# Kernel optimization log

Measured on AMD Instinct MI355X. Metric: run time of the kernel, lower is better.

## Reference

```python
import jax, jax.numpy as jnp
import numpy as np


def conv2d(x, w, bias, stride=1, pad=0, groups=1):
    out = jax.lax.conv_general_dilated(
        x, w, (stride, stride), [(pad, pad), (pad, pad)],
        dimension_numbers=("NCHW", "OIHW", "NCHW"), feature_group_count=groups)
    return out + bias[None, :, None, None]


PATCHSIZE = [(4, 4), (8, 8)]
NEG = jnp.float32(-1e9)


def setup_inputs() -> dict:
    key = jax.random.key(0)
    ks = jax.random.split(key, 24)
    d = 128
    s = 0.05
    inp = {
        "x": jax.random.normal(ks[0], (16, d, 64, 64), jnp.float32),
        "m": jax.random.uniform(ks[1], (16, 1, 64, 64), jnp.float32),
        "depth_map": jax.random.normal(ks[2], (16, 1, 256, 256), jnp.float32),
        "wq": jax.random.normal(ks[3], (d, d, 1, 1), jnp.float32) * s,
        "bq": jax.random.normal(ks[4], (d,), jnp.float32) * s,
        "wk": jax.random.normal(ks[5], (d, d, 1, 1), jnp.float32) * s,
        "bk": jax.random.normal(ks[6], (d,), jnp.float32) * s,
        "wv": jax.random.normal(ks[7], (d, d, 1, 1), jnp.float32) * s,
        "bv": jax.random.normal(ks[8], (d,), jnp.float32) * s,
        "wvle": jax.random.normal(ks[9], (d, 1, 3, 3), jnp.float32) * s,  # depthwise
        "bvle": jax.random.normal(ks[10], (d,), jnp.float32) * s,
        "wd1": jax.random.normal(ks[11], (d, 1, 3, 3), jnp.float32) * s,
        "bd1": jax.random.normal(ks[12], (d,), jnp.float32) * s,
        "wd2": jax.random.normal(ks[13], (1, d, 3, 3), jnp.float32) * s,
        "bd2": jax.random.normal(ks[14], (1,), jnp.float32) * s,
        "wo": jax.random.normal(ks[15], (d, d, 3, 3), jnp.float32) * s,
        "bo": jax.random.normal(ks[16], (d,), jnp.float32) * s,
        "b": 2,
        "c": 128,
    }
    return inp


def _forward(x, m, depth_map, wq, bq, wk, bk, wv, bv, wvle, bvle,
             wd1, bd1, wd2, bd2, wo, bo, b, c):
    bt, _, h, w = x.shape
    t = bt // b
    d_k = c // len(PATCHSIZE)

    q_all = conv2d(x, wq, bq)
    k_all = conv2d(x, wk, bk)
    v_all = conv2d(x, wv, bv) + conv2d(x, wvle, bvle, pad=1, groups=c)
    d1 = jax.nn.relu(conv2d(depth_map, wd1, bd1, stride=2, pad=1))
    _depth = jax.nn.relu(conv2d(d1, wd2, bd2, stride=2, pad=1))  # (bt,1,h,w)

    outs = []
    for i, (width, height) in enumerate(PATCHSIZE):
        out_w, out_h = w // width, h // height
        L = t * out_h * out_w

        def patch(z, ch):
            # (b*t, ch, h, w) -> (b, L, ch*height*width)
            z = z.reshape(b, t, ch, out_h, height, out_w, width)
            return z.transpose(0, 1, 3, 5, 2, 4, 6).reshape(b, L, ch * height * width)

        mask = jnp.mean(patch(m, 1), -1) > 0.5            # (b, L) per-key mask
        dsort = jnp.sort(patch(_depth, 1), -1)            # (b, L, height*width)
        hw = height * width
        dmin, dmed, dmax = dsort[..., 0], dsort[..., (hw - 1) // 2], dsort[..., -1]

        q = patch(q_all[:, i * d_k:(i + 1) * d_k], d_k)
        k_ = patch(k_all[:, i * d_k:(i + 1) * d_k], d_k)
        v = patch(v_all[:, i * d_k:(i + 1) * d_k], d_k)

        scale = 1.0 / jnp.sqrt(jnp.float32(q.shape[-1]))
        s = jnp.einsum("bqd,bkd->bqk", q, k_) * scale     # shared QK^T

        def head(dbias):
            ss = s * jax.nn.sigmoid(dbias)[:, None, :]
            ss = jnp.where(mask[:, None, :], NEG, ss)
            return jnp.einsum("bqk,bkd->bqd", jax.nn.softmax(ss, -1), v)

        y = (head(dmed) + head(dmax) + head(dmin)) / 3.0
        y = y.reshape(b, t, out_h, out_w, d_k, height, width)
        y = y.transpose(0, 1, 4, 2, 5, 3, 6).reshape(bt, d_k, h, w)
        outs.append(y)

    out = jnp.concatenate(outs, 1)
    out = conv2d(out, wo, bo, pad=1)
    out = jnp.where(out >= 0, out, 0.2 * out)  # LeakyReLU(0.2)
    return out


def reference(x, m, depth_map, wq, bq, wk, bk, wv, bv, wvle, bvle,
              wd1, bd1, wd2, bd2, wo, bo, b, c):
    out = _forward(x, m, depth_map, wq, bq, wk, bk, wv, bv, wvle, bvle,
                   wd1, bd1, wd2, bd2, wo, bo, b, c)
    return (out, depth_map)
```

## Files before the change

kernel.cpp:

```cpp
#include <hip/hip_runtime.h>
#include <cmath>

typedef unsigned short u16;
typedef __attribute__((ext_vector_type(8))) __bf16 bf16x8;
typedef __attribute__((ext_vector_type(4))) float f32x4;

constexpr int Bb = 2, Tt = 8, Dc = 128, PIX = 4096;

__device__ inline u16 f2bf(float f) {
    unsigned u = __builtin_bit_cast(unsigned, f);
    u += 0x7fffu + ((u >> 16) & 1u);
    return (u16)(u >> 16);
}
__device__ inline float bf2f(u16 h) {
    unsigned u = ((unsigned)h) << 16;
    return __builtin_bit_cast(float, u);
}

#define GLOAD16(gp, lp) __builtin_amdgcn_global_load_lds( \
    (const __attribute__((address_space(1))) void*)(const void*)(gp), \
    (__attribute__((address_space(3))) void*)(void*)(lp), 16, 0, 0)

__device__ inline void mfma_chunk(const u16* lAs, const u16* lBs, int wave, int lane,
                                  f32x4 (&acc)[4][4])
{
    const int wm = (wave >> 1) * 64, wn = (wave & 1) * 64;
    const int fr = lane & 15;
    const int q4 = lane >> 4;
    const int sw = (q4 ^ ((fr >> 1) & 3)) * 8;
    bf16x8 av[4], bv[4];
#pragma unroll
    for (int i = 0; i < 4; ++i) av[i] = *(const bf16x8*)&lAs[(wm + i * 16 + fr) * 32 + sw];
#pragma unroll
    for (int j = 0; j < 4; ++j) bv[j] = *(const bf16x8*)&lBs[(wn + j * 16 + fr) * 32 + sw];
#pragma unroll
    for (int i = 0; i < 4; ++i)
#pragma unroll
        for (int j = 0; j < 4; ++j)
            acc[i][j] = __builtin_amdgcn_mfma_f32_16x16x32_bf16(av[i], bv[j], acc[i][j], 0, 0, 0);
}

__device__ inline void stage_chunk(const u16* ga0, const u16* ga1,
                                   const u16* gb0, const u16* gb1,
                                   int kb, u16* lA, u16* lB, int wave)
{
    GLOAD16(ga0 + kb * 32, lA + wave * 1024);
    GLOAD16(ga1 + kb * 32, lA + wave * 1024 + 512);
    GLOAD16(gb0 + kb * 32, lB + wave * 1024);
    GLOAD16(gb1 + kb * 32, lB + wave * 1024 + 512);
}

__device__ inline void mfma_nt(const u16* A, int ldkA, const u16* B, int ldkB,
                               int kChunks, int wave, int lane,
                               u16* lAs, u16* lBs, f32x4 (&acc)[4][4])
{
    const int r = lane >> 2;
    const int kq8 = ((lane & 3) ^ ((r >> 1) & 3)) * 8;
    const u16* ga0 = A + (size_t)(wave * 32 + r) * ldkA + kq8;
    const u16* ga1 = ga0 + (size_t)16 * ldkA;
    const u16* gb0 = B + (size_t)(wave * 32 + r) * ldkB + kq8;
    const u16* gb1 = gb0 + (size_t)16 * ldkB;
    stage_chunk(ga0, ga1, gb0, gb1, 0, lAs, lBs, wave);
    __syncthreads();
    for (int kb = 0; kb < kChunks; ++kb) {
        if (kb + 1 < kChunks) {
            const int nx = ((kb + 1) & 1) * 4096;
            stage_chunk(ga0, ga1, gb0, gb1, kb + 1, lAs + nx, lBs + nx, wave);
        }
        const int cur = (kb & 1) * 4096;
        mfma_chunk(lAs + cur, lBs + cur, wave, lane, acc);
        __syncthreads();
    }
}

__global__ void k_prep(const float* __restrict__ wq, const float* __restrict__ wk,
                       const float* __restrict__ wv, const float* __restrict__ wo,
                       u16* __restrict__ Wqkv, u16* __restrict__ WoT)
{
    int idx = blockIdx.x * 256 + threadIdx.x;
    if (idx < 49152) {
        const float* w = idx < 16384 ? wq : (idx < 32768 ? wk : wv);
        Wqkv[idx] = f2bf(w[idx & 16383]);
    }
    int j = idx - 49152;
    if (j >= 0 && j < 147456) {
        int tap = j / 16384, rem = j % 16384;
        WoT[j] = f2bf(wo[(size_t)rem * 9 + tap]);
    }
}

__global__ __launch_bounds__(256) void k_xt(const float* __restrict__ x, u16* __restrict__ Xt)
{
    __shared__ float ls[128 * 65];
    const int n = blockIdx.y, pix0 = blockIdx.x * 64;
#pragma unroll
    for (int rep = 0; rep < 32; ++rep) {
        int idx = rep * 256 + threadIdx.x;
        int cin = idx >> 6, p = idx & 63;
        ls[cin * 65 + p] = x[((size_t)n * Dc + cin) * PIX + pix0 + p];
    }
    __syncthreads();
#pragma unroll
    for (int rep = 0; rep < 32; ++rep) {
        int idx = rep * 256 + threadIdx.x;
        int p = idx >> 7, cin = idx & 127;
        Xt[((size_t)n * PIX + pix0 + p) * Dc + cin] = f2bf(ls[cin * 65 + p]);
    }
}

__global__ __launch_bounds__(256) void k_qkv_mfma(const u16* __restrict__ Wqkv,
                                                  const u16* __restrict__ Xt,
                                                  const float* __restrict__ bq,
                                                  const float* __restrict__ bk,
                                                  const float* __restrict__ bv,
                                                  u16* __restrict__ Qp0, u16* __restrict__ Kp0,
                                                  u16* __restrict__ Qp1, u16* __restrict__ Kp1,
                                                  u16* __restrict__ v_bf)
{
    __shared__ u16 lAs[8192], lBs[8192];
    const int tid = threadIdx.x, wave = tid >> 6, lane = tid & 63;
    const int mt = blockIdx.y, n = blockIdx.z, px0 = blockIdx.x * 128;
    f32x4 acc[4][4];
#pragma unroll
    for (int i = 0; i < 4; ++i)
#pragma unroll
        for (int j = 0; j < 4; ++j) acc[i][j] = (f32x4){0.f, 0.f, 0.f, 0.f};
    mfma_nt(Wqkv + (size_t)mt * 128 * 128, 128,
            Xt + ((size_t)n * PIX + px0) * 128, 128, 4, wave, lane, lAs, lBs, acc);
    const int wm = (wave >> 1) * 64, wn = (wave & 1) * 64;
    const int rb = (lane >> 4) * 4, cb = lane & 15;
    const int bi = n >> 3, ti = n & 7;
    if (mt < 2) {
        const float* bp = (mt == 0) ? bq : bk;
        u16* d0 = (mt == 0) ? Qp0 : Kp0;
        u16* d1 = (mt == 0) ? Qp1 : Kp1;
#pragma unroll
        for (int i = 0; i < 4; ++i)
#pragma unroll
            for (int reg = 0; reg < 4; ++reg) {
                int c = wm + i * 16 + rb + reg;
                float bias = bp[c];
#pragma unroll
                for (int j = 0; j < 4; ++j) {
                    int pix = px0 + wn + j * 16 + cb;
                    int y = pix >> 6, x = pix & 63;
                    u16 val = f2bf(acc[i][j][reg] + bias);
                    if (c < 64) {
                        int l = ti * 256 + (y >> 2) * 16 + (x >> 2);
                        int f = c * 16 + (y & 3) * 4 + (x & 3);
                        d0[((size_t)bi * 2048 + l) * 1024 + f] = val;
                    } else {
                        int l = ti * 64 + (y >> 3) * 8 + (x >> 3);
                        int f = (c - 64) * 64 + (y & 7) * 8 + (x & 7);
                        d1[((size_t)bi * 512 + l) * 4096 + f] = val;
                    }
                }
            }
    } else {
#pragma unroll
        for (int i = 0; i < 4; ++i)
#pragma unroll
            for (int reg = 0; reg < 4; ++reg) {
                int c = wm + i * 16 + rb + reg;
                float bias = bv[c];
#pragma unroll
                for (int j = 0; j < 4; ++j) {
                    int pix = px0 + wn + j * 16 + cb;
                    v_bf[((size_t)n * Dc + c) * PIX + pix] = f2bf(acc[i][j][reg] + bias);
                }
            }
    }
}

__global__ __launch_bounds__(256) void k_fuse(const float* __restrict__ X,
                                              const float* __restrict__ wvle,
                                              const float* __restrict__ bvle,
                                              const u16* __restrict__ v_bf,
                                              u16* __restrict__ Vt0,
                                              u16* __restrict__ Vt1,
                                              const float* __restrict__ dm,
                                              const float* __restrict__ wd1,
                                              const float* __restrict__ bd1,
                                              const float* __restrict__ wd2,
                                              float* __restrict__ part)
{
    __shared__ float ls[4096];
    __shared__ u16 lv[64 * 65];
    const int id = blockIdx.x;
    const int sub = id >> 1;
    const int tid = threadIdx.x;
    if ((id & 1) == 0) {
        const int c = sub & 127, n = sub >> 7;
        const int bi = n >> 3, ti = n & 7;
        const float* xp = X + ((size_t)n * Dc + c) * PIX;
#pragma unroll
        for (int r = 0; r < 4; ++r)
            *(float4*)&ls[r * 1024 + tid * 4] = *(const float4*)&xp[r * 1024 + tid * 4];
        __syncthreads();
        float w[9];
#pragma unroll
        for (int t = 0; t < 9; ++t) w[t] = wvle[c * 9 + t];
        const float bias = bvle[c];
        const int x = tid & 63, y0 = (tid >> 6) * 16;
        const bool xl = (x > 0), xr = (x < 63);
        const u16* vp = v_bf + ((size_t)n * Dc + c) * PIX;
#pragma unroll
        for (int r = 0; r < 16; ++r) {
            int y = y0 + r;
            float s = bias;
#pragma unroll
            for (int ky = 0; ky < 3; ++ky) {
                int yy = y + ky - 1;
                if (yy < 0 || yy > 63) continue;
                const float* row = &ls[yy * 64];
                float m   = row[x];
                float lv_ = xl ? row[x - 1] : 0.f;
                float rv  = xr ? row[x + 1] : 0.f;
                s += w[ky * 3 + 0] * lv_ + w[ky * 3 + 1] * m + w[ky * 3 + 2] * rv;
            }
            lv[y * 65 + x] = f2bf(bf2f(vp[y * 64 + x]) + s);
        }
        __syncthreads();
        if (c < 64) {
            const int fsub = tid >> 4;
            const int py = fsub >> 2, px = fsub & 3;
            const int oh = tid & 15;
            u16 buf[16];
#pragma unroll
            for (int ow = 0; ow < 16; ++ow)
                buf[ow] = lv[(oh * 4 + py) * 65 + ow * 4 + px];
            size_t dst = ((size_t)bi * 1024 + (c * 16 + fsub)) * 2048 + ti * 256 + oh * 16;
            *(uint4*)&Vt0[dst]     = *(const uint4*)&buf[0];
            *(uint4*)&Vt0[dst + 8] = *(const uint4*)&buf[8];
        } else {
            const int fsub = tid >> 2;
            const int py = fsub >> 3, px = fsub & 7;
            const int l0 = (tid & 3) * 16;
            u16 buf[16];
#pragma unroll
            for (int e = 0; e < 16; ++e) {
                int l = l0 + e, oh = l >> 3, ow = l & 7;
                buf[e] = lv[(oh * 8 + py) * 65 + ow * 8 + px];
            }
            size_t dst = ((size_t)bi * 4096 + ((c - 64) * 64 + fsub)) * 512 + ti * 64 + l0;
            *(uint4*)&Vt1[dst]     = *(const uint4*)&buf[0];
            *(uint4*)&Vt1[dst + 8] = *(const uint4*)&buf[8];
        }
    } else {
        const int tile = sub & 15, n = (sub >> 4) & 15, cs = sub >> 8;
        const int ty = tid >> 4, tx = tid & 15;
        const int y = (tile >> 2) * 16 + ty;
        const int x = (tile & 3) * 16 + tx;
        const float* dmp = dm + (size_t)n * 65536;
        const int gc0 = 4 * x - 4;
        const bool vy = (y > 0), vx = (x > 0);
        const int c0 = cs * 16;
        float acc = 0.f;
#pragma unroll 1
        for (int jy = 0; jy < 3; ++jy) {
            float rw[3][7];
#pragma unroll
            for (int rr = 0; rr < 3; ++rr) {
                const int gr = 4 * y - 3 + 2 * jy + rr;
                const float* rp = dmp + gr * 256 + gc0;
                const bool rok = (gr >= 0);
                float4 va = (rok && x > 0) ? *(const float4*)rp
                                           : make_float4(0.f, 0.f, 0.f, 0.f);
                float4 vb = rok ? *(const float4*)(rp + 4)
                                : make_float4(0.f, 0.f, 0.f, 0.f);
                rw[rr][0] = va.y; rw[rr][1] = va.z; rw[rr][2] = va.w;
                rw[rr][3] = vb.x; rw[rr][4] = vb.y; rw[rr][5] = vb.z; rw[rr][6] = vb.w;
            }
#pragma unroll
            for (int rr = 0; rr < 3; ++rr)
#pragma unroll
                for (int i = 0; i < 7; ++i) asm volatile("" : "+v"(rw[rr][i]));
            const bool oky = (jy > 0) || vy;
#pragma unroll 2
            for (int cc = 0; cc < 16; ++cc) {
                const int c = c0 + cc;
                const float* w1 = wd1 + c * 9;
                const float* w2 = wd2 + c * 9 + jy * 3;
                const float b1 = bd1[c];
#pragma unroll
                for (int jx = 0; jx < 3; ++jx) {
                    float s = b1;
#pragma unroll
                    for (int ky = 0; ky < 3; ++ky)
#pragma unroll
                        for (int kx = 0; kx < 3; ++kx)
                            s += w1[ky * 3 + kx] * rw[ky][2 * jx + kx];
                    s = fmaxf(s, 0.f);
                    const bool ok = oky && ((jx > 0) || vx);
                    acc += w2[jx] * (ok ? s : 0.f);
                }
            }
        }
        part[((size_t)cs * 16 + n) * PIX + y * 64 + x] = acc;
    }
}

__global__ void k_dfin(const float* __restrict__ part, const float* __restrict__ bd2,
                       float* __restrict__ dep)
{
    int idx = blockIdx.x * 256 + threadIdx.x;
    float s = bd2[0];
#pragma unroll
    for (int cg = 0; cg < 8; ++cg) s += part[(size_t)cg * 65536 + idx];
    dep[idx] = fmaxf(s, 0.f);
}

template<int PS>
__global__ __launch_bounds__(256) void k_stats2(const float* __restrict__ mI,
                                                const float* __restrict__ dep,
                                                float* __restrict__ maskf,
                                                float* __restrict__ smed,
                                                float* __restrict__ smaxA,
                                                float* __restrict__ sminA,
                                                int outn, int L)
{
    constexpr int HW = PS * PS;
    constexpr int TPB = 256 / HW;
    const int tok = blockIdx.x * TPB + threadIdx.x / HW;
    const int el  = threadIdx.x % HW;
    if (tok >= Bb * L) return;
    const int bi = tok / L, l = tok % L;
    const int ti = l / (outn * outn); const int rem = l % (outn * outn);
    const int oh = rem / outn, ow = rem % outn;
    const int n = bi * Tt + ti;
    const int py = el / PS, px = el % PS;
    const size_t off = (size_t)n * PIX + (size_t)(oh * PS + py) * 64 + ow * PS + px;
    const float mv = mI[off];
    const float dv = dep[off];
    float msum = mv, vmin = dv, vmax = dv;
#pragma unroll
    for (int o = HW / 2; o > 0; o >>= 1) {
        msum += __shfl_xor(msum, o);
        vmin = fminf(vmin, __shfl_xor(vmin, o));
        vmax = fmaxf(vmax, __shfl_xor(vmax, o));
    }
    const int gbase = (threadIdx.x & 63) & ~(HW - 1);
    int cl = 0, ce = 0;
#pragma unroll
    for (int b2 = 0; b2 < HW; ++b2) {
        float vb = __shfl(dv, gbase + b2);
        cl += (vb < dv);
        ce += (vb == dv);
    }
    constexpr int kk = (HW - 1) / 2;
    if (el == 0) {
        maskf[tok] = (msum / (float)HW > 0.5f) ? 1.f : 0.f;
        smaxA[tok] = 1.f / (1.f + __expf(-vmax));
        sminA[tok] = 1.f / (1.f + __expf(-vmin));
    }
    if (cl <= kk && kk < cl + ce)
        smed[tok] = 1.f / (1.f + __expf(-dv));
}

__global__ __launch_bounds__(256) void k_qkT_mfma(const u16* __restrict__ Qp,
                                                  const u16* __restrict__ Kp,
                                                  u16* __restrict__ S,
                                                  int L, int F, int ksplit, float scale)
{
    __shared__ u16 lAs[8192], lBs[8192];
    const int tid = threadIdx.x, wave = tid >> 6, lane = tid & 63;
    const int bi = blockIdx.z / ksplit, ks = blockIdx.z % ksplit;
    const int kf = F / ksplit;
    f32x4 acc[4][4];
#pragma unroll
    for (int i = 0; i < 4; ++i)
#pragma unroll
        for (int j = 0; j < 4; ++j) acc[i][j] = (f32x4){0.f, 0.f, 0.f, 0.f};
    mfma_nt(Qp + (size_t)bi * L * F + (size_t)blockIdx.y * 128 * F + (size_t)ks * kf, F,
            Kp + (size_t)bi * L * F + (size_t)blockIdx.x * 128 * F + (size_t)ks * kf, F,
            kf / 32, wave, lane, lAs, lBs, acc);
    const int wm = (wave >> 1) * 64, wn = (wave & 1) * 64;
    const int rb = (lane >> 4) * 4, cb = lane & 15;
    u16* Cp = S + ((size_t)ks * Bb + bi) * L * L;
#pragma unroll
    for (int i = 0; i < 4; ++i)
#pragma unroll
        for (int reg = 0; reg < 4; ++reg) {
            int gm = blockIdx.y * 128 + wm + i * 16 + rb + reg;
#pragma unroll
            for (int j = 0; j < 4; ++j) {
                int gn = blockIdx.x * 128 + wn + j * 16 + cb;
                Cp[(size_t)gm * L + gn] = f2bf(acc[i][j][reg] * scale);
            }
        }
}

__device__ inline float blockMax(float v, float* sh) {
#pragma unroll
    for (int o = 32; o > 0; o >>= 1) v = fmaxf(v, __shfl_down(v, o));
    __syncthreads();
    if ((threadIdx.x & 63) == 0) sh[threadIdx.x >> 6] = v;
    __syncthreads();
    return fmaxf(fmaxf(sh[0], sh[1]), fmaxf(sh[2], sh[3]));
}
__device__ inline float blockSum(float v, float* sh) {
#pragma unroll
    for (int o = 32; o > 0; o >>= 1) v += __shfl_down(v, o);
    __syncthreads();
    if ((threadIdx.x & 63) == 0) sh[threadIdx.x >> 6] = v;
    __syncthreads();
    return sh[0] + sh[1] + sh[2] + sh[3];
}

template<int NPAIR, int NSPLIT>
__global__ __launch_bounds__(256) void k_softmax(const u16* __restrict__ S,
                                                 u16* __restrict__ Pb,
                                                 const float* __restrict__ maskf,
                                                 const float* __restrict__ smed,
                                                 const float* __restrict__ smaxA,
                                                 const float* __restrict__ sminA,
                                                 int L)
{
    __shared__ float sred[4];
    const int bi = blockIdx.y, q = blockIdx.x;
    const size_t pstr = (size_t)Bb * L * L;
    const u16* row = S + (size_t)bi * L * L + (size_t)q * L;
    u16* prow = Pb + (size_t)bi * L * L + (size_t)q * L;
    const float* mk  = maskf + bi * L;
    const float* s0p = smed  + bi * L;
    const float* s1p = smaxA + bi * L;
    const float* s2p = sminA + bi * L;
    const int tid = threadIdx.x;
    float a0[2 * NPAIR], a1[2 * NPAIR], a2[2 * NPAIR];
    float m0 = -3.4e38f, m1 = -3.4e38f, m2 = -3.4e38f;
#pragma unroll
    for (int e = 0; e < NPAIR; ++e) {
        int k = e * 512 + tid * 2;
        unsigned u = *(const unsigned*)&row[k];
        float sva = bf2f((u16)(u & 0xffffu));
        float svb = bf2f((u16)(u >> 16));
#pragma unroll
        for (int s2 = 1; s2 < NSPLIT; ++s2) {
            unsigned w = *(const unsigned*)&row[(size_t)s2 * pstr + k];
            sva += bf2f((u16)(w & 0xffffu));
            svb += bf2f((u16)(w >> 16));
        }
        float2 mv  = *(const float2*)&mk[k];
        float2 p0  = *(const float2*)&s0p[k];
        float2 p1  = *(const float2*)&s1p[k];
        float2 p2  = *(const float2*)&s2p[k];
        bool ma = mv.x > 0.5f, mb = mv.y > 0.5f;
        float v0a = ma ? -1e9f : sva * p0.x, v0b = mb ? -1e9f : svb * p0.y;
        float v1a = ma ? -1e9f : sva * p1.x, v1b = mb ? -1e9f : svb * p1.y;
        float v2a = ma ? -1e9f : sva * p2.x, v2b = mb ? -1e9f : svb * p2.y;
        a0[2 * e] = v0a; a0[2 * e + 1] = v0b;
        a1[2 * e] = v1a; a1[2 * e + 1] = v1b;
        a2[2 * e] = v2a; a2[2 * e + 1] = v2b;
        m0 = fmaxf(m0, fmaxf(v0a, v0b));
        m1 = fmaxf(m1, fmaxf(v1a, v1b));
        m2 = fmaxf(m2, fmaxf(v2a, v2b));
    }
    m0 = blockMax(m0, sred); m1 = blockMax(m1, sred); m2 = blockMax(m2, sred);
    float l0 = 0.f, l1 = 0.f, l2 = 0.f;
#pragma unroll
    for (int e = 0; e < 2 * NPAIR; ++e) {
        a0[e] = __expf(a0[e] - m0); l0 += a0[e];
        a1[e] = __expf(a1[e] - m1); l1 += a1[e];
        a2[e] = __expf(a2[e] - m2); l2 += a2[e];
    }
    l0 = blockSum(l0, sred); l1 = blockSum(l1, sred); l2 = blockSum(l2, sred);
    float c0 = 1.f / (3.f * l0), c1 = 1.f / (3.f * l1), c2 = 1.f / (3.f * l2);
#pragma unroll
    for (int e = 0; e < NPAIR; ++e) {
        int k = e * 512 + tid * 2;
        u16 oa = f2bf(a0[2 * e] * c0 + a1[2 * e] * c1 + a2[2 * e] * c2);
        u16 ob = f2bf(a0[2 * e + 1] * c0 + a1[2 * e + 1] * c1 + a2[2 * e + 1] * c2);
        unsigned pk = (unsigned)oa | ((unsigned)ob << 16);
        *(unsigned*)&prow[k] = pk;
    }
}

__global__ __launch_bounds__(256) void k_pv_mfma(const u16* __restrict__ Pb,
                                                 const u16* __restrict__ Vt,
                                                 u16* __restrict__ Yp,
                                                 int L, int F, int ksplit)
{
    __shared__ u16 lAs[8192], lBs[8192];
    const int tid = threadIdx.x, wave = tid >> 6, lane = tid & 63;
    const int bi = blockIdx.z / ksplit, ks = blockIdx.z % ksplit;
    const int kf = L / ksplit;
    f32x4 acc[4][4];
#pragma unroll
    for (int i = 0; i < 4; ++i)
#pragma unroll
        for (int j = 0; j < 4; ++j) acc[i][j] = (f32x4){0.f, 0.f, 0.f, 0.f};
    mfma_nt(Pb + (size_t)bi * L * L + (size_t)blockIdx.y * 128 * L + (size_t)ks * kf, L,
            Vt + (size_t)bi * F * L + (size_t)blockIdx.x * 128 * L + (size_t)ks * kf, L,
            kf / 32, wave, lane, lAs, lBs, acc);
    const int wm = (wave >> 1) * 64, wn = (wave & 1) * 64;
    const int rb = (lane >> 4) * 4, cb = lane & 15;
    u16* Cp = Yp + ((size_t)(ks * Bb + bi) * L) * F;
#pragma unroll
    for (int i = 0; i < 4; ++i)
#pragma unroll
        for (int reg = 0; reg < 4; ++reg) {
            int gm = blockIdx.y * 128 + wm + i * 16 + rb + reg;
#pragma unroll
            for (int j = 0; j < 4; ++j) {
                int gn = blockIdx.x * 128 + wn + j * 16 + cb;
                Cp[(size_t)gm * F + gn] = f2bf(acc[i][j][reg]);
            }
        }
}

template<int NSPLIT>
__global__ void k_unpatch(const u16* __restrict__ Yp, u16* __restrict__ catbT,
                          int ps, int outn, int L, int F, int cbase)
{
    size_t idx = (size_t)blockIdx.x * 256 + threadIdx.x;
    size_t total = (size_t)Bb * L * F / 4;
    if (idx >= total) return;
    const size_t pstr = (size_t)Bb * L * F;
    int f0 = (int)((idx * 4) % F);
    size_t t2 = (idx * 4) / F;
    int l = (int)(t2 % L);
    int bi = (int)(t2 / L);
    size_t off = ((size_t)bi * L + l) * F + f0;
    float s[4] = {0.f, 0.f, 0.f, 0.f};
#pragma unroll
    for (int sp = 0; sp < NSPLIT; ++sp) {
        uint2 u = *(const uint2*)&Yp[(size_t)sp * pstr + off];
        s[0] += bf2f((u16)(u.x & 0xffffu));
        s[1] += bf2f((u16)(u.x >> 16));
        s[2] += bf2f((u16)(u.y & 0xffffu));
        s[3] += bf2f((u16)(u.y >> 16));
    }
    int hw = ps * ps;
    int c = cbase + f0 / hw, r0 = f0 % hw;
    int ti = l / (outn * outn); int rem = l % (outn * outn);
    int oh = rem / outn, ow = rem % outn;
    int n = bi * Tt + ti;
    int py = r0 / ps, px = r0 % ps;
    size_t base = ((size_t)n * PIX + (size_t)(oh * ps + py) * 64 + ow * ps + px) * Dc + c;
#pragma unroll
    for (int e = 0; e < 4; ++e)
        catbT[base + (size_t)e * Dc] = f2bf(s[e]);
}

__global__ __launch_bounds__(256) void k_conv_mfma(const u16* __restrict__ catbT,
                                                   const u16* __restrict__ WoT,
                                                   const u16* __restrict__ zp,
                                                   u16* __restrict__ Cpart)
{
    __shared__ u16 lAs[8192], lBs[8192];
    const int tid = threadIdx.x, wave = tid >> 6, lane = tid & 63;
    const int pix0 = blockIdx.x * 128;
    const int sp = blockIdx.y;
    const int r = lane >> 2;
    const int kq8 = ((lane & 3) ^ ((r >> 1) & 3)) * 8;
    int yb[2], xb[2], nn[2];
#pragma unroll
    for (int s = 0; s < 2; ++s) {
        int pg = pix0 + wave * 32 + r + s * 16;
        nn[s] = pg >> 12; yb[s] = (pg >> 6) & 63; xb[s] = pg & 63;
    }
    const u16* gb_base = WoT + (size_t)(wave * 32 + r) * 128 + kq8;

    auto stage = [&](int tt, int hb) {
        const int t = sp * 18 + tt;
        const int tap = t >> 2, kc = t & 3;
        const int dy = tap / 3 - 1, dx = tap % 3 - 1;
        const u16* ga[2];
#pragma unroll
        for (int s = 0; s < 2; ++s) {
            int y = yb[s] + dy, xx = xb[s] + dx;
            bool ok = ((unsigned)y < 64u) && ((unsigned)xx < 64u);
            ga[s] = ok ? catbT + (((size_t)(nn[s] << 12) + y * 64 + xx) << 7) + kq8 + kc * 32 : zp;
        }
        const u16* gb = gb_base + tap * 16384 + kc * 32;
        GLOAD16(ga[0],     lAs + hb * 4096 + wave * 1024);
        GLOAD16(ga[1],     lAs + hb * 4096 + wave * 1024 + 512);
        GLOAD16(gb,        lBs + hb * 4096 + wave * 1024);
        GLOAD16(gb + 2048, lBs + hb * 4096 + wave * 1024 + 512);
    };

    f32x4 acc[4][4];
#pragma unroll
    for (int i = 0; i < 4; ++i)
#pragma unroll
        for (int j = 0; j < 4; ++j) acc[i][j] = (f32x4){0.f, 0.f, 0.f, 0.f};

    stage(0, 0);
    __syncthreads();
    for (int tt = 0; tt < 18; ++tt) {
        if (tt + 1 < 18) stage(tt + 1, (tt + 1) & 1);
        const int cur = (tt & 1) * 4096;
        mfma_chunk(lAs + cur, lBs + cur, wave, lane, acc);
        __syncthreads();
    }

    const int wm = (wave >> 1) * 64, wn = (wave & 1) * 64;
    const int rb = (lane >> 4) * 4, cb = lane & 15;
    u16* Cp = Cpart + (size_t)sp * 8388608;
#pragma unroll
    for (int i = 0; i < 4; ++i)
#pragma unroll
        for (int reg = 0; reg < 4; ++reg) {
            int gm = pix0 + wm + i * 16 + rb + reg;
#pragma unroll
            for (int j = 0; j < 4; ++j) {
                int gn = wn + j * 16 + cb;
                Cp[(size_t)gm * 128 + gn] = f2bf(acc[i][j][reg]);
            }
        }
}

__global__ __launch_bounds__(256) void k_cfin(const u16* __restrict__ Cpart,
                                              const float* __restrict__ bo,
                                              float* __restrict__ outp)
{
    const int pg0 = blockIdx.x * 64;
    const int lane = threadIdx.x & 63, wv = threadIdx.x >> 6;
    const int pix = pg0 + lane;
    const int n = pix >> 12, p = pix & 4095;
    const u16* r0 = Cpart + (size_t)pix * 128 + wv * 32;
    const u16* r1 = r0 + 8388608;
#pragma unroll
    for (int c4 = 0; c4 < 8; ++c4) {
        uint2 a = *(const uint2*)(r0 + c4 * 4);
        uint2 b = *(const uint2*)(r1 + c4 * 4);
        float s[4];
        s[0] = bf2f((u16)(a.x & 0xffffu)) + bf2f((u16)(b.x & 0xffffu));
        s[1] = bf2f((u16)(a.x >> 16))     + bf2f((u16)(b.x >> 16));
        s[2] = bf2f((u16)(a.y & 0xffffu)) + bf2f((u16)(b.y & 0xffffu));
        s[3] = bf2f((u16)(a.y >> 16))     + bf2f((u16)(b.y >> 16));
#pragma unroll
        for (int e = 0; e < 4; ++e) {
            int cout = wv * 32 + c4 * 4 + e;
            float v = s[e] + bo[cout];
            v = (v >= 0.f) ? v : 0.2f * v;
            outp[((size_t)n * Dc + cout) * PIX + p] = v;
        }
    }
}

extern "C" void kernel_launch(void* const* d_in, const int* in_sizes, int n_in,
                              void* d_out, int out_size, void* d_ws, size_t ws_size,
                              hipStream_t stream)
{
    (void)in_sizes; (void)n_in; (void)out_size; (void)ws_size;
    const float* x    = (const float*)d_in[0];
    const float* mI   = (const float*)d_in[1];
    const float* dmap = (const float*)d_in[2];
    const float* wq   = (const float*)d_in[3];
    const float* bq   = (const float*)d_in[4];
    const float* wk   = (const float*)d_in[5];
    const float* bk   = (const float*)d_in[6];
    const float* wv   = (const float*)d_in[7];
    const float* bv   = (const float*)d_in[8];
    const float* wvle = (const float*)d_in[9];
    const float* bvle = (const float*)d_in[10];
    const float* wd1  = (const float*)d_in[11];
    const float* bd1  = (const float*)d_in[12];
    const float* wd2  = (const float*)d_in[13];
    const float* bd2  = (const float*)d_in[14];
    const float* wo   = (const float*)d_in[15];
    const float* bo   = (const float*)d_in[16];

    char* w8 = (char*)d_ws;
    u16*   v_bf  = (u16*)(w8);
    u16*   Xt    = (u16*)(w8 + 0x1000000);
    u16*   catbT = (u16*)(w8 + 0x2000000);
    u16*   Qp0   = (u16*)(w8 + 0x3000000);
    u16*   Kp0   = (u16*)(w8 + 0x3800000);
    u16*   Qp1   = (u16*)(w8 + 0x4000000);
    u16*   Kp1   = (u16*)(w8 + 0x4800000);
    u16*   Vt0   = (u16*)(w8 + 0x5000000);
    u16*   Sb    = (u16*)(w8 + 0x5800000);
    u16*   Pb    = (u16*)(w8 + 0x7800000);
    u16*   Yp    = (u16*)(w8 + 0x8800000);
    u16*   Cpart = (u16*)(w8 + 0x5800000);
    float* dep   = (float*)(w8 + 0xA800000);
    float* maskf = (float*)(w8 + 0xA840000);
    float* smed  = (float*)(w8 + 0xA844000);
    float* smaxA = (float*)(w8 + 0xA848000);
    float* sminA = (float*)(w8 + 0xA84C000);
    u16*   Wqkv  = (u16*)(w8 + 0xA850000);
    u16*   WoT   = (u16*)(w8 + 0xA868000);
    u16*   zp    = (u16*)(w8 + 0xA8B0000);
    float* part  = (float*)(w8 + 0xA8C0000);
    u16*   Vt1   = (u16*)(w8 + 0xAAC0000);
    float* outp  = (float*)d_out;

    hipMemcpyAsync(outp + 8388608, dmap, (size_t)16 * 65536 * sizeof(float),
                   hipMemcpyDeviceToDevice, stream);
    hipMemsetAsync(zp, 0, 256, stream);

    dim3 blk(256);
    k_prep<<<dim3(768), blk, 0, stream>>>(wq, wk, wv, wo, Wqkv, WoT);
    k_xt<<<dim3(64, 16), blk, 0, stream>>>(x, Xt);
    k_qkv_mfma<<<dim3(32, 3, 16), blk, 0, stream>>>(Wqkv, Xt, bq, bk, bv,
                                                    Qp0, Kp0, Qp1, Kp1, v_bf);

    k_fuse<<<dim3(4096), blk, 0, stream>>>(x, wvle, bvle, v_bf, Vt0, Vt1,
                                           dmap, wd1, bd1, wd2, part);
    k_dfin<<<dim3(256), blk, 0, stream>>>(part, bd2, dep);

    for (int i = 0; i < 2; ++i) {
        const int ps = (i == 0) ? 4 : 8;
        const int outn = 64 / ps;
        const int L = Tt * outn * outn;
        const int F = 64 * ps * ps;
        const float scale = 1.0f / sqrtf((float)F);
        const int ksplit  = (i == 0) ? 2 : 16;
        const int pvsplit = 4;
        const u16* Qp = (i == 0) ? Qp0 : Qp1;
        const u16* Kp = (i == 0) ? Kp0 : Kp1;
        const u16* Vt = (i == 0) ? Vt0 : Vt1;

        if (i == 0) k_stats2<4><<<dim3(Bb * L * 16 / 256), blk, 0, stream>>>(mI, dep, maskf, smed, smaxA, sminA, outn, L);
        else        k_stats2<8><<<dim3(Bb * L * 64 / 256), blk, 0, stream>>>(mI, dep, maskf, smed, smaxA, sminA, outn, L);

        k_qkT_mfma<<<dim3(L / 128, L / 128, Bb * ksplit), blk, 0, stream>>>(Qp, Kp, Sb, L, F, ksplit, scale);

        if (i == 0) k_softmax<4, 2><<<dim3(L, Bb), blk, 0, stream>>>(Sb, Pb, maskf, smed, smaxA, sminA, L);
        else        k_softmax<1, 16><<<dim3(L, Bb), blk, 0, stream>>>(Sb, Pb, maskf, smed, smaxA, sminA, L);

        k_pv_mfma<<<dim3(F / 128, L / 128, Bb * pvsplit), blk, 0, stream>>>(Pb, Vt, Yp, L, F, pvsplit);

        const int pgrid = (int)(((size_t)Bb * L * F / 4 + 255) / 256);
        k_unpatch<4><<<dim3(pgrid), blk, 0, stream>>>(Yp, catbT, ps, outn, L, F, i * 64);
    }

    k_conv_mfma<<<dim3(512, 2), blk, 0, stream>>>(catbT, WoT, zp, Cpart);
    k_cfin<<<dim3(1024), blk, 0, stream>>>(Cpart, bo, outp);
}
```

Before: 395.9 us.

## Merge both patch-size attention branches into single horizontally fused launches

Each stage of the two patch-size attention branches (stats, QK^T, softmax, PV, unpatch) now runs as one combined launch that dispatches on block index, instead of a per-branch loop of separate launches. The weight-prep and input-transpose kernels are also merged into one launch. The PV split-K factor drops from 4 to 2, so fewer partial outputs are written and reduced in unpatch. This cuts launch count and lets the small 8x8-patch grids share the GPU with the 4x4 work. In exchange, separate per-branch buffers are needed, so the workspace is re-laid out with more aliasing, and PV has less parallelism per branch.

Measured after the change: 386.3 us. -2.4%, faster.

```diff
diff --git a/kernel.cpp b/kernel.cpp
--- a/kernel.cpp
+++ b/kernel.cpp
@@ -73,26 +73,57 @@
     }
 }
 
-__global__ void k_prep(const float* __restrict__ wq, const float* __restrict__ wk,
-                       const float* __restrict__ wv, const float* __restrict__ wo,
-                       u16* __restrict__ Wqkv, u16* __restrict__ WoT)
-{
-    int idx = blockIdx.x * 256 + threadIdx.x;
-    if (idx < 49152) {
-        const float* w = idx < 16384 ? wq : (idx < 32768 ? wk : wv);
-        Wqkv[idx] = f2bf(w[idx & 16383]);
-    }
-    int j = idx - 49152;
-    if (j >= 0 && j < 147456) {
-        int tap = j / 16384, rem = j % 16384;
-        WoT[j] = f2bf(wo[(size_t)rem * 9 + tap]);
-    }
-}
-
-__global__ __launch_bounds__(256) void k_xt(const float* __restrict__ x, u16* __restrict__ Xt)
+__device__ inline void gemm_body(const u16* A, const u16* B, int ldk, int kChunks,
+                                 u16* Cp, int ldc, float scale,
+                                 int bx, int by, int tid, u16* lAs, u16* lBs)
+{
+    const int wave = tid >> 6, lane = tid & 63;
+    f32x4 acc[4][4];
+#pragma unroll
+    for (int i = 0; i < 4; ++i)
+#pragma unroll
+        for (int j = 0; j < 4; ++j) acc[i][j] = (f32x4){0.f, 0.f, 0.f, 0.f};
+    mfma_nt(A, ldk, B, ldk, kChunks, wave, lane, lAs, lBs, acc);
+    const int wm = (wave >> 1) * 64, wn = (wave & 1) * 64;
+    const int rb = (lane >> 4) * 4, cb = lane & 15;
+#pragma unroll
+    for (int i = 0; i < 4; ++i)
+#pragma unroll
+        for (int reg = 0; reg < 4; ++reg) {
+            int gm = by * 128 + wm + i * 16 + rb + reg;
+#pragma unroll
+            for (int j = 0; j < 4; ++j) {
+                int gn = bx * 128 + wn + j * 16 + cb;
+                Cp[(size_t)gm * ldc + gn] = f2bf(acc[i][j][reg] * scale);
+            }
+        }
+}
+
+__global__ __launch_bounds__(256) void k_px(const float* __restrict__ wq,
+                                            const float* __restrict__ wk,
+                                            const float* __restrict__ wv,
+                                            const float* __restrict__ wo,
+                                            u16* __restrict__ Wqkv, u16* __restrict__ WoT,
+                                            const float* __restrict__ x,
+                                            u16* __restrict__ Xt)
 {
     __shared__ float ls[128 * 65];
-    const int n = blockIdx.y, pix0 = blockIdx.x * 64;
+    const int id = blockIdx.x;
+    if (id < 768) {
+        int idx = id * 256 + threadIdx.x;
+        if (idx < 49152) {
+            const float* w = idx < 16384 ? wq : (idx < 32768 ? wk : wv);
+            Wqkv[idx] = f2bf(w[idx & 16383]);
+        }
+        int j = idx - 49152;
+        if (j >= 0 && j < 147456) {
+            int tap = j / 16384, rem = j % 16384;
+            WoT[j] = f2bf(wo[(size_t)rem * 9 + tap]);
+        }
+        return;
+    }
+    const int b2 = id - 768;
+    const int n = b2 >> 6, pix0 = (b2 & 63) * 64;
 #pragma unroll
     for (int rep = 0; rep < 32; ++rep) {
         int idx = rep * 256 + threadIdx.x;
@@ -311,17 +342,15 @@
 }
 
 template<int PS>
-__global__ __launch_bounds__(256) void k_stats2(const float* __restrict__ mI,
-                                                const float* __restrict__ dep,
-                                                float* __restrict__ maskf,
-                                                float* __restrict__ smed,
-                                                float* __restrict__ smaxA,
-                                                float* __restrict__ sminA,
-                                                int outn, int L)
+__device__ inline void stats_body(int sid, const float* __restrict__ mI,
+                                  const float* __restrict__ dep,
+                                  float* __restrict__ maskf, float* __restrict__ smed,
+                                  float* __restrict__ smaxA, float* __restrict__ sminA,
+                                  int outn, int L)
 {
     constexpr int HW = PS * PS;
     constexpr int TPB = 256 / HW;
-    const int tok = blockIdx.x * TPB + threadIdx.x / HW;
+    const int tok = sid * TPB + (int)threadIdx.x / HW;
     const int el  = threadIdx.x % HW;
     if (tok >= Bb * L) return;
     const int bi = tok / L, l = tok % L;
@@ -357,37 +386,44 @@
         smed[tok] = 1.f / (1.f + __expf(-dv));
 }
 
-__global__ __launch_bounds__(256) void k_qkT_mfma(const u16* __restrict__ Qp,
-                                                  const u16* __restrict__ Kp,
-                                                  u16* __restrict__ S,
-                                                  int L, int F, int ksplit, float scale)
+__global__ __launch_bounds__(256) void k_stats(const float* __restrict__ mI,
+                                               const float* __restrict__ dep,
+                                               float* __restrict__ mk0, float* __restrict__ s00,
+                                               float* __restrict__ s10, float* __restrict__ s20,
+                                               float* __restrict__ mk1, float* __restrict__ s01,
+                                               float* __restrict__ s11, float* __restrict__ s21)
+{
+    const int id = blockIdx.x;
+    if (id < 256) stats_body<4>(id, mI, dep, mk0, s00, s10, s20, 16, 2048);
+    else          stats_body<8>(id - 256, mI, dep, mk1, s01, s11, s21, 8, 512);
+}
+
+__global__ __launch_bounds__(256) void k_qkT2(const u16* __restrict__ Qp0,
+                                              const u16* __restrict__ Kp0,
+                                              u16* __restrict__ Sb0,
+                                              const u16* __restrict__ Qp1,
+                                              const u16* __restrict__ Kp1,
+                                              u16* __restrict__ Sb1)
 {
     __shared__ u16 lAs[8192], lBs[8192];
-    const int tid = threadIdx.x, wave = tid >> 6, lane = tid & 63;
-    const int bi = blockIdx.z / ksplit, ks = blockIdx.z % ksplit;
-    const int kf = F / ksplit;
-    f32x4 acc[4][4];
-#pragma unroll
-    for (int i = 0; i < 4; ++i)
-#pragma unroll
-        for (int j = 0; j < 4; ++j) acc[i][j] = (f32x4){0.f, 0.f, 0.f, 0.f};
-    mfma_nt(Qp + (size_t)bi * L * F + (size_t)blockIdx.y * 128 * F + (size_t)ks * kf, F,
-            Kp + (size_t)bi * L * F + (size_t)blockIdx.x * 128 * F + (size_t)ks * kf, F,
-            kf / 32, wave, lane, lAs, lBs, acc);
-    const int wm = (wave >> 1) * 64, wn = (wave & 1) * 64;
-    const int rb = (lane >> 4) * 4, cb = lane & 15;
-    u16* Cp = S + ((size_t)ks * Bb + bi) * L * L;
-#pragma unroll
-    for (int i = 0; i < 4; ++i)
-#pragma unroll
-        for (int reg = 0; reg < 4; ++reg) {
-            int gm = blockIdx.y * 128 + wm + i * 16 + rb + reg;
-#pragma unroll
-            for (int j = 0; j < 4; ++j) {
-                int gn = blockIdx.x * 128 + wn + j * 16 + cb;
-                Cp[(size_t)gm * L + gn] = f2bf(acc[i][j][reg] * scale);
-            }
-        }
+    int id = blockIdx.x;
+    const int tid = threadIdx.x;
+    if (id < 1024) {
+        const int bx = id & 15, by = (id >> 4) & 15, z = id >> 8;
+        const int bi = z >> 1, ks = z & 1;
+        const u16* A = Qp0 + (size_t)bi * 2048 * 1024 + (size_t)by * 128 * 1024 + (size_t)ks * 512;
+        const u16* B = Kp0 + (size_t)bi * 2048 * 1024 + (size_t)bx * 128 * 1024 + (size_t)ks * 512;
+        u16* Cp = Sb0 + ((size_t)ks * Bb + bi) * 2048 * 2048;
+        gemm_body(A, B, 1024, 16, Cp, 2048, 0.03125f, bx, by, tid, lAs, lBs);
+    } else {
+        id -= 1024;
+        const int bx = id & 3, by = (id >> 2) & 3, z = id >> 4;
+        const int bi = z >> 4, ks = z & 15;
+        const u16* A = Qp1 + (size_t)bi * 512 * 4096 + (size_t)by * 128 * 4096 + (size_t)ks * 256;
+        const u16* B = Kp1 + (size_t)bi * 512 * 4096 + (size_t)bx * 128 * 4096 + (size_t)ks * 256;
+        u16* Cp = Sb1 + ((size_t)ks * Bb + bi) * 512 * 512;
+        gemm_body(A, B, 4096, 8, Cp, 512, 0.015625f, bx, by, tid, lAs, lBs);
+    }
 }
 
 __device__ inline float blockMax(float v, float* sh) {
@@ -408,16 +444,13 @@
 }
 
 template<int NPAIR, int NSPLIT>
-__global__ __launch_bounds__(256) void k_softmax(const u16* __restrict__ S,
-                                                 u16* __restrict__ Pb,
-                                                 const float* __restrict__ maskf,
-                                                 const float* __restrict__ smed,
-                                                 const float* __restrict__ smaxA,
-                                                 const float* __restrict__ sminA,
-                                                 int L)
-{
-    __shared__ float sred[4];
-    const int bi = blockIdx.y, q = blockIdx.x;
+__device__ inline void softmax_body(const u16* __restrict__ S, u16* __restrict__ Pb,
+                                    const float* __restrict__ maskf,
+                                    const float* __restrict__ smed,
+                                    const float* __restrict__ smaxA,
+                                    const float* __restrict__ sminA,
+                                    int L, int bi, int q, float* sred)
+{
     const size_t pstr = (size_t)Bb * L * L;
     const u16* row = S + (size_t)bi * L * L + (size_t)q * L;
     u16* prow = Pb + (size_t)bi * L * L + (size_t)q * L;
@@ -475,44 +508,58 @@
     }
 }
 
-__global__ __launch_bounds__(256) void k_pv_mfma(const u16* __restrict__ Pb,
-                                                 const u16* __restrict__ Vt,
-                                                 u16* __restrict__ Yp,
-                                                 int L, int F, int ksplit)
+__global__ __launch_bounds__(256) void k_sm2(const u16* __restrict__ Sb0, u16* __restrict__ Pb0,
+                                             const float* __restrict__ mk0, const float* __restrict__ s00,
+                                             const float* __restrict__ s10, const float* __restrict__ s20,
+                                             const u16* __restrict__ Sb1, u16* __restrict__ Pb1,
+                                             const float* __restrict__ mk1, const float* __restrict__ s01,
+                                             const float* __restrict__ s11, const float* __restrict__ s21)
+{
+    __shared__ float sred[4];
+    int id = blockIdx.x;
+    if (id < 4096) {
+        const int bi = id >> 11, q = id & 2047;
+        softmax_body<4, 2>(Sb0, Pb0, mk0, s00, s10, s20, 2048, bi, q, sred);
+    } else {
+        id -= 4096;
+        const int bi = id >> 9, q = id & 511;
+        softmax_body<1, 16>(Sb1, Pb1, mk1, s01, s11, s21, 512, bi, q, sred);
+    }
+}
+
+__global__ __launch_bounds__(256) void k_pv2(const u16* __restrict__ Pb0,
+                                             const u16* __restrict__ Vt0,
+                                             u16* __restrict__ Yp0,
+                                             const u16* __restrict__ Pb1,
+                                             const u16* __restrict__ Vt1,
+                                             u16* __restrict__ Yp1)
 {
     __shared__ u16 lAs[8192], lBs[8192];
-    const int tid = threadIdx.x, wave = tid >> 6, lane = tid & 63;
-    const int bi = blockIdx.z / ksplit, ks = blockIdx.z % ksplit;
-    const int kf = L / ksplit;
-    f32x4 acc[4][4];
-#pragma unroll
-    for (int i = 0; i < 4; ++i)
-#pragma unroll
-        for (int j = 0; j < 4; ++j) acc[i][j] = (f32x4){0.f, 0.f, 0.f, 0.f};
-    mfma_nt(Pb + (size_t)bi * L * L + (size_t)blockIdx.y * 128 * L + (size_t)ks * kf, L,
-            Vt + (size_t)bi * F * L + (size_t)blockIdx.x * 128 * L + (size_t)ks * kf, L,
-            kf / 32, wave, lane, lAs, lBs, acc);
-    const int wm = (wave >> 1) * 64, wn = (wave & 1) * 64;
-    const int rb = (lane >> 4) * 4, cb = lane & 15;
-    u16* Cp = Yp + ((size_t)(ks * Bb + bi) * L) * F;
-#pragma unroll
-    for (int i = 0; i < 4; ++i)
-#pragma unroll
-        for (int reg = 0; reg < 4; ++reg) {
-            int gm = blockIdx.y * 128 + wm + i * 16 + rb + reg;
-#pragma unroll
-            for (int j = 0; j < 4; ++j) {
-                int gn = blockIdx.x * 128 + wn + j * 16 + cb;
-                Cp[(size_t)gm * F + gn] = f2bf(acc[i][j][reg]);
-            }
-        }
+    int id = blockIdx.x;
+    const int tid = threadIdx.x;
+    if (id < 512) {
+        const int bx = id & 7, by = (id >> 3) & 15, z = id >> 7;
+        const int bi = z >> 1, ks = z & 1;
+        const u16* A = Pb0 + (size_t)bi * 2048 * 2048 + (size_t)by * 128 * 2048 + (size_t)ks * 1024;
+        const u16* B = Vt0 + (size_t)bi * 1024 * 2048 + (size_t)bx * 128 * 2048 + (size_t)ks * 1024;
+        u16* Cp = Yp0 + ((size_t)ks * Bb + bi) * 2048 * 1024;
+        gemm_body(A, B, 2048, 32, Cp, 1024, 1.0f, bx, by, tid, lAs, lBs);
+    } else {
+        id -= 512;
+        const int bx = id & 31, by = (id >> 5) & 3, z = id >> 7;
+        const int bi = z >> 1, ks = z & 1;
+        const u16* A = Pb1 + (size_t)bi * 512 * 512 + (size_t)by * 128 * 512 + (size_t)ks * 256;
+        const u16* B = Vt1 + (size_t)bi * 4096 * 512 + (size_t)bx * 128 * 512 + (size_t)ks * 256;
+        u16* Cp = Yp1 + ((size_t)ks * Bb + bi) * 512 * 4096;
+        gemm_body(A, B, 512, 8, Cp, 4096, 1.0f, bx, by, tid, lAs, lBs);
+    }
 }
 
 template<int NSPLIT>
-__global__ void k_unpatch(const u16* __restrict__ Yp, u16* __restrict__ catbT,
-                          int ps, int outn, int L, int F, int cbase)
-{
-    size_t idx = (size_t)blockIdx.x * 256 + threadIdx.x;
+__device__ inline void unp_body(int sid, const u16* __restrict__ Yp, u16* __restrict__ catbT,
+                                int ps, int outn, int L, int F, int cbase)
+{
+    size_t idx = (size_t)sid * 256 + threadIdx.x;
     size_t total = (size_t)Bb * L * F / 4;
     if (idx >= total) return;
     const size_t pstr = (size_t)Bb * L * F;
@@ -540,6 +587,14 @@
 #pragma unroll
     for (int e = 0; e < 4; ++e)
         catbT[base + (size_t)e * Dc] = f2bf(s[e]);
+}
+
+__global__ void k_unp2(const u16* __restrict__ Yp0, const u16* __restrict__ Yp1,
+                       u16* __restrict__ catbT)
+{
+    const int id = blockIdx.x;
+    if (id < 4096) unp_body<2>(id, Yp0, catbT, 4, 16, 2048, 1024, 0);
+    else           unp_body<2>(id - 4096, Yp1, catbT, 8, 8, 512, 4096, 64);
 }
 
 __global__ __launch_bounds__(256) void k_conv_mfma(const u16* __restrict__ catbT,
@@ -665,26 +720,33 @@
     char* w8 = (char*)d_ws;
     u16*   v_bf  = (u16*)(w8);
     u16*   Xt    = (u16*)(w8 + 0x1000000);
+    u16*   Yp0   = (u16*)(w8);
     u16*   catbT = (u16*)(w8 + 0x2000000);
     u16*   Qp0   = (u16*)(w8 + 0x3000000);
     u16*   Kp0   = (u16*)(w8 + 0x3800000);
     u16*   Qp1   = (u16*)(w8 + 0x4000000);
     u16*   Kp1   = (u16*)(w8 + 0x4800000);
     u16*   Vt0   = (u16*)(w8 + 0x5000000);
-    u16*   Sb    = (u16*)(w8 + 0x5800000);
-    u16*   Pb    = (u16*)(w8 + 0x7800000);
-    u16*   Yp    = (u16*)(w8 + 0x8800000);
-    u16*   Cpart = (u16*)(w8 + 0x5800000);
-    float* dep   = (float*)(w8 + 0xA800000);
-    float* maskf = (float*)(w8 + 0xA840000);
-    float* smed  = (float*)(w8 + 0xA844000);
-    float* smaxA = (float*)(w8 + 0xA848000);
-    float* sminA = (float*)(w8 + 0xA84C000);
-    u16*   Wqkv  = (u16*)(w8 + 0xA850000);
-    u16*   WoT   = (u16*)(w8 + 0xA868000);
-    u16*   zp    = (u16*)(w8 + 0xA8B0000);
-    float* part  = (float*)(w8 + 0xA8C0000);
-    u16*   Vt1   = (u16*)(w8 + 0xAAC0000);
+    u16*   Vt1   = (u16*)(w8 + 0x5800000);
+    u16*   Sb0   = (u16*)(w8 + 0x6000000);
+    u16*   Yp1   = (u16*)(w8 + 0x6000000);
+    u16*   Cpart = (u16*)(w8 + 0x6000000);
+    u16*   Sb1   = (u16*)(w8 + 0x8000000);
+    u16*   Pb0   = (u16*)(w8 + 0x9000000);
+    u16*   Pb1   = (u16*)(w8 + 0xA000000);
+    float* part  = (float*)(w8 + 0xA100000);
+    float* dep   = (float*)(w8 + 0xA300000);
+    float* maskf = (float*)(w8 + 0xA340000);
+    float* smed  = (float*)(w8 + 0xA344000);
+    float* smaxA = (float*)(w8 + 0xA348000);
+    float* sminA = (float*)(w8 + 0xA34C000);
+    float* mk1   = (float*)(w8 + 0xA350000);
+    float* sm1a  = (float*)(w8 + 0xA354000);
+    float* sm1b  = (float*)(w8 + 0xA358000);
+    float* sm1c  = (float*)(w8 + 0xA35C000);
+    u16*   Wqkv  = (u16*)(w8 + 0xA360000);
+    u16*   WoT   = (u16*)(w8 + 0xA378000);
+    u16*   zp    = (u16*)(w8 + 0xA3C0000);
     float* outp  = (float*)d_out;
 
     hipMemcpyAsync(outp + 8388608, dmap, (size_t)16 * 65536 * sizeof(float),
@@ -692,8 +754,7 @@
     hipMemsetAsync(zp, 0, 256, stream);
 
     dim3 blk(256);
-    k_prep<<<dim3(768), blk, 0, stream>>>(wq, wk, wv, wo, Wqkv, WoT);
-    k_xt<<<dim3(64, 16), blk, 0, stream>>>(x, Xt);
+    k_px<<<dim3(1792), blk, 0, stream>>>(wq, wk, wv, wo, Wqkv, WoT, x, Xt);
     k_qkv_mfma<<<dim3(32, 3, 16), blk, 0, stream>>>(Wqkv, Xt, bq, bk, bv,
                                                     Qp0, Kp0, Qp1, Kp1, v_bf);
 
@@ -701,31 +762,13 @@
                                            dmap, wd1, bd1, wd2, part);
     k_dfin<<<dim3(256), blk, 0, stream>>>(part, bd2, dep);
 
-    for (int i = 0; i < 2; ++i) {
-        const int ps = (i == 0) ? 4 : 8;
-        const int outn = 64 / ps;
-        const int L = Tt * outn * outn;
-        const int F = 64 * ps * ps;
-        const float scale = 1.0f / sqrtf((float)F);
-        const int ksplit  = (i == 0) ? 2 : 16;
-        const int pvsplit = 4;
-        const u16* Qp = (i == 0) ? Qp0 : Qp1;
-        const u16* Kp = (i == 0) ? Kp0 : Kp1;
-        const u16* Vt = (i == 0) ? Vt0 : Vt1;
-
-        if (i == 0) k_stats2<4><<<dim3(Bb * L * 16 / 256), blk, 0, stream>>>(mI, dep, maskf, smed, smaxA, sminA, outn, L);
-        else        k_stats2<8><<<dim3(Bb * L * 64 / 256), blk, 0, stream>>>(mI, dep, maskf, smed, smaxA, sminA, outn, L);
-
-        k_qkT_mfma<<<dim3(L / 128, L / 128, Bb * ksplit), blk, 0, stream>>>(Qp, Kp, Sb, L, F, ksplit, scale);
-
-        if (i == 0) k_softmax<4, 2><<<dim3(L, Bb), blk, 0, stream>>>(Sb, Pb, maskf, smed, smaxA, sminA, L);
-        else        k_softmax<1, 16><<<dim3(L, Bb), blk, 0, stream>>>(Sb, Pb, maskf, smed, smaxA, sminA, L);
-
-        k_pv_mfma<<<dim3(F / 128, L / 128, Bb * pvsplit), blk, 0, stream>>>(Pb, Vt, Yp, L, F, pvsplit);
-
-        const int pgrid = (int)(((size_t)Bb * L * F / 4 + 255) / 256);
-        k_unpatch<4><<<dim3(pgrid), blk, 0, stream>>>(Yp, catbT, ps, outn, L, F, i * 64);
-    }
+    k_stats<<<dim3(512), blk, 0, stream>>>(mI, dep, maskf, smed, smaxA, sminA,
+                                           mk1, sm1a, sm1b, sm1c);
+    k_qkT2<<<dim3(1536), blk, 0, stream>>>(Qp0, Kp0, Sb0, Qp1, Kp1, Sb1);
+    k_sm2<<<dim3(5120), blk, 0, stream>>>(Sb0, Pb0, maskf, smed, smaxA, sminA,
+                                          Sb1, Pb1, mk1, sm1a, sm1b, sm1c);
+    k_pv2<<<dim3(1024), blk, 0, stream>>>(Pb0, Vt0, Yp0, Pb1, Vt1, Yp1);
+    k_unp2<<<dim3(8192), blk, 0, stream>>>(Yp0, Yp1, catbT);
 
     k_conv_mfma<<<dim3(512, 2), blk, 0, stream>>>(catbT, WoT, zp, Cpart);
     k_cfin<<<dim3(1024), blk, 0, stream>>>(Cpart, bo, outp);
```
